# Kernel tuning notes

Measured on AMD Instinct MI355X. Metric: run time of the kernel, lower is better.

## Reference

```python
import jax, jax.numpy as jnp
import numpy as np

N, E = 50000, 800000
HID, EDGE_DIM, HEADS = 128, 16, 4
C = HID // HEADS  # 32
NEG_SLOPE = 0.2  # GATv2Conv default negative_slope


def setup_inputs() -> dict:
    key = jax.random.key(0)
    ks = jax.random.split(key, 16)
    def glorot(k, shape):
        fan_in = shape[0]
        return jax.random.normal(k, shape, jnp.float32) / np.sqrt(fan_in)
    return {
        "x": jax.random.normal(ks[0], (N, HID), jnp.float32),
        "edge_index": jax.random.randint(ks[1], (2, E), 0, N, jnp.int64 if jax.config.jax_enable_x64 else jnp.int32),
        "edge_attr": jax.random.normal(ks[2], (E, EDGE_DIM), jnp.float32),
        # GATv2Conv params (lin_l, lin_r with bias; lin_edge bias-free; att; final bias)
        "Wl": glorot(ks[3], (HID, HID)),
        "bl": jnp.zeros((HID,), jnp.float32),
        "Wr": glorot(ks[4], (HID, HID)),
        "br": jnp.zeros((HID,), jnp.float32),
        "We": glorot(ks[5], (EDGE_DIM, HID)),
        "att": glorot(ks[6], (HEADS, C)),
        "bias_gat": jnp.zeros((HID,), jnp.float32),
        # RMSNorm weights
        "w_norm1": jnp.ones((HID,), jnp.float32),
        "w_norm2": jnp.ones((HID,), jnp.float32),
        # FFN params
        "ffn_w1": glorot(ks[7], (HID, 4 * HID)),
        "ffn_b1": jnp.zeros((4 * HID,), jnp.float32),
        "ffn_w2": glorot(ks[8], (4 * HID, HID)),
        "ffn_b2": jnp.zeros((HID,), jnp.float32),
    }


def rmsnorm(x, w):
    # torch.nn.RMSNorm with eps=None -> eps = finfo(dtype).eps
    eps = jnp.finfo(x.dtype).eps
    ms = jnp.mean(x * x, axis=-1, keepdims=True)
    return x * jax.lax.rsqrt(ms + eps) * w


def gatv2_conv(x, edge_index, edge_attr, Wl, bl, Wr, br, We, att, bias_gat):
    n = x.shape[0]
    h, c = att.shape
    xl = (x @ Wl + bl).reshape(n, h, c)   # source-side transform (x_j)
    xr = (x @ Wr + br).reshape(n, h, c)   # target-side transform (x_i)
    src, dst = edge_index[0], edge_index[1]
    e = (edge_attr @ We).reshape(-1, h, c)
    m = xl[src] + xr[dst] + e                       # [E, H, C] per-edge message pre-activation
    s = jnp.where(m > 0, m, NEG_SLOPE * m)          # LeakyReLU(0.2)
    logits = jnp.einsum('ehc,hc->eh', s, att)       # [E, H]
    # scatter-softmax over edges grouped by target node
    lmax = jax.ops.segment_max(logits, dst, num_segments=n)
    ex = jnp.exp(logits - lmax[dst])
    den = jax.ops.segment_sum(ex, dst, num_segments=n)
    alpha = ex / (den[dst] + 1e-16)                 # PyG softmax denominator guard
    out = jax.ops.segment_sum(alpha[..., None] * xl[src], dst, num_segments=n)
    return out.reshape(n, h * c) + bias_gat


def reference(x, edge_index, edge_attr, Wl, bl, Wr, br, We, att, bias_gat,
              w_norm1, w_norm2, ffn_w1, ffn_b1, ffn_w2, ffn_b2):
    x_attn = gatv2_conv(x, edge_index, edge_attr, Wl, bl, Wr, br, We, att, bias_gat)
    h = rmsnorm(x + x_attn, w_norm1)
    f = jax.nn.gelu(h @ ffn_w1 + ffn_b1, approximate=False) @ ffn_w2 + ffn_b2
    return rmsnorm(h + f, w_norm2)
```

## Files before the change

kernel.cpp:

```cpp
#include <hip/hip_runtime.h>

#define NN 50000
#define EE 800000

typedef unsigned short u16;

#define OFF_EAH  0u
#define OFF_XLH  6400000u
#define OFF_XRH  9600000u
#define OFF_SE   12800000u
#define OFF_CNT  14400000u
#define OFF_OFS  14450000u
#define OFF_WLRT 16000000u
#define OFF_W1T  16016384u
#define OFF_W2T  16049152u

#define RMS_EPS 1.1920928955078125e-7f

typedef float f32x4v __attribute__((ext_vector_type(4)));
typedef short s16x8 __attribute__((ext_vector_type(8)));
typedef _Float16 h16x2 __attribute__((ext_vector_type(2)));
typedef __fp16   g16x2 __attribute__((ext_vector_type(2)));

__device__ __forceinline__ f32x4v mfma16(s16x8 a, s16x8 b, f32x4v c) {
  return __builtin_amdgcn_mfma_f32_16x16x32_bf16(a, b, c, 0, 0, 0);
}
__device__ __forceinline__ u16 f2b(float f) {
  unsigned int u = __float_as_uint(f);
  unsigned int r = (u + 0x7fffu + ((u >> 16) & 1u)) >> 16;
  return (u16)r;
}
__device__ __forceinline__ u16 f2h(float f) {
  union { _Float16 h; u16 u; } x; x.h = (_Float16)f; return x.u;
}
__device__ __forceinline__ h16x2 pk(float a, float b) {
  union { g16x2 g; h16x2 h; } u; u.g = __builtin_amdgcn_cvt_pkrtz(a, b); return u.h;
}
__device__ __forceinline__ h16x2 u2h(unsigned int u) {
  union { unsigned int i; h16x2 h; } x; x.i = u; return x.h;
}
__device__ __forceinline__ unsigned int h2u(h16x2 h) {
  union { unsigned int i; h16x2 h; } x; x.h = h; return x.i;
}
__device__ __forceinline__ float fdot2(h16x2 a, h16x2 b, float c) {
  union { h16x2 h; g16x2 g; } ua, ub; ua.h = a; ub.h = b;
  return __builtin_amdgcn_fdot2(ua.g, ub.g, c, false);
}
__device__ __forceinline__ s16x8 ld_bf16x8_f32(const float* p) {
  float4 v0 = *(const float4*)p;
  float4 v1 = *(const float4*)(p + 4);
  s16x8 r;
  r[0] = (short)f2b(v0.x); r[1] = (short)f2b(v0.y);
  r[2] = (short)f2b(v0.z); r[3] = (short)f2b(v0.w);
  r[4] = (short)f2b(v1.x); r[5] = (short)f2b(v1.y);
  r[6] = (short)f2b(v1.z); r[7] = (short)f2b(v1.w);
  return r;
}
__device__ __forceinline__ int readlane_i32(int v, int lane) {
  return __builtin_amdgcn_readlane(v, lane);
}
__device__ __forceinline__ float gelu_fast(float x) {
  float x2 = x * x;
  float y = x * fmaf(0.07135481283f, x2, 1.5957691216f);
  float e = __expf(-y);
  return x * __builtin_amdgcn_rcpf(1.0f + e);
}

__global__ __launch_bounds__(256) void k_prep(const float* __restrict__ Wl, const float* __restrict__ Wr,
    const float* __restrict__ W1, const float* __restrict__ W2,
    int* __restrict__ cnt, u16* __restrict__ wlrt, u16* __restrict__ w1t, u16* __restrict__ w2t)
{
  int i = blockIdx.x * 256 + threadIdx.x;
  if (i < NN) cnt[i] = 0;
  if (i < 32768) {
    int n = i >> 7, k = i & 127;
    float v = (n < 128) ? Wl[k * 128 + n] : Wr[k * 128 + (n - 128)];
    wlrt[i] = f2b(v);
  }
  {
    int n = i >> 7, k = i & 127;
    w1t[i] = f2b(W1[k * 512 + n]);
  }
  {
    int n = i >> 9, k = i & 511;
    w2t[i] = f2b(W2[k * 128 + n]);
  }
}

__global__ __launch_bounds__(256) void k_hist(const int* __restrict__ ei, const float* __restrict__ eattr,
    int* __restrict__ cnt, unsigned int* __restrict__ eah)
{
  int e = blockIdx.x * 256 + threadIdx.x;
  if (e < EE) {
    atomicAdd(&cnt[ei[EE + e]], 1);
    const float4* src = (const float4*)(eattr + (size_t)e * 16);
    float4 v0 = src[0], v1 = src[1], v2 = src[2], v3 = src[3];
    uint4 o0, o1;
    o0.x = h2u(pk(v0.x, v0.y));
    o0.y = h2u(pk(v0.z, v0.w));
    o0.z = h2u(pk(v1.x, v1.y));
    o0.w = h2u(pk(v1.z, v1.w));
    o1.x = h2u(pk(v2.x, v2.y));
    o1.y = h2u(pk(v2.z, v2.w));
    o1.z = h2u(pk(v3.x, v3.y));
    o1.w = h2u(pk(v3.z, v3.w));
    uint4* dst = (uint4*)(eah + (size_t)e * 8);
    dst[0] = o0; dst[1] = o1;
  }
}

__global__ __launch_bounds__(1024) void k_scan(const int* __restrict__ cnt,
    int* __restrict__ offs, int* __restrict__ pos)
{
  __shared__ int wsum[16];
  __shared__ int carry_s;
  int tid = threadIdx.x, lane = tid & 63, wv = tid >> 6;
  if (tid == 0) carry_s = 0;
  __syncthreads();
  for (int base = 0; base < NN; base += 1024) {
    int i = base + tid;
    int v = (i < NN) ? cnt[i] : 0;
    int x = v;
#pragma unroll
    for (int ofs = 1; ofs < 64; ofs <<= 1) {
      int y = __shfl_up(x, ofs);
      if (lane >= ofs) x += y;
    }
    if (lane == 63) wsum[wv] = x;
    __syncthreads();
    if (wv == 0) {
      int s = (lane < 16) ? wsum[lane] : 0;
#pragma unroll
      for (int ofs = 1; ofs < 16; ofs <<= 1) {
        int y = __shfl_up(s, ofs);
        if (lane >= ofs) s += y;
      }
      if (lane < 16) wsum[lane] = s;
    }
    __syncthreads();
    int wbase = (wv > 0) ? wsum[wv - 1] : 0;
    int incl = x + wbase + carry_s;
    if (i < NN) { offs[i + 1] = incl; pos[i] = incl - v; }
    if (base == 0 && tid == 0) offs[0] = 0;
    __syncthreads();
    if (tid == 1023) carry_s = incl;
    __syncthreads();
  }
}

__global__ __launch_bounds__(256) void k_permute(const int* __restrict__ ei,
    int* __restrict__ pos, int2* __restrict__ se)
{
  int e = blockIdx.x * 256 + threadIdx.x;
  if (e < EE) {
    int slot = atomicAdd(&pos[ei[EE + e]], 1);
    se[slot] = make_int2(ei[e], e);
  }
}

__global__ __launch_bounds__(256) void k1_mfma(const float* __restrict__ x, const u16* __restrict__ wlrt,
    const float* __restrict__ bl, const float* __restrict__ br,
    u16* __restrict__ xlh, u16* __restrict__ xrh)
{
  int tid = threadIdx.x;
  int w = tid >> 6, lane = tid & 63;
  int quad = lane >> 4, l16 = lane & 15;
  int row0 = blockIdx.x * 32;
  int ko = quad * 8;
  f32x4v acc[2][4];
#pragma unroll
  for (int mt = 0; mt < 2; ++mt)
#pragma unroll
    for (int nt = 0; nt < 4; ++nt) acc[mt][nt] = (f32x4v){0.f, 0.f, 0.f, 0.f};
#pragma unroll
  for (int ks = 0; ks < 4; ++ks) {
    int k0 = ks * 32 + ko;
    s16x8 a[2];
#pragma unroll
    for (int mt = 0; mt < 2; ++mt) {
      int row = row0 + mt * 16 + l16; if (row >= NN) row = NN - 1;
      a[mt] = ld_bf16x8_f32(x + row * 128 + k0);
    }
#pragma unroll
    for (int nt = 0; nt < 4; ++nt) {
      int col = w * 64 + nt * 16 + l16;
      s16x8 b = *(const s16x8*)(wlrt + col * 128 + k0);
      acc[0][nt] = mfma16(a[0], b, acc[0][nt]);
      acc[1][nt] = mfma16(a[1], b, acc[1][nt]);
    }
  }
#pragma unroll
  for (int nt = 0; nt < 4; ++nt) {
    int col = w * 64 + nt * 16 + l16;
    bool isl = col < 128;
    float bias = isl ? bl[col] : br[col - 128];
    u16* dst = isl ? xlh : xrh;
    int cc = isl ? col : col - 128;
#pragma unroll
    for (int mt = 0; mt < 2; ++mt)
#pragma unroll
      for (int r = 0; r < 4; ++r) {
        int row = row0 + mt * 16 + quad * 4 + r;
        if (row < NN) dst[row * 128 + cc] = f2h(acc[mt][nt][r] + bias);
      }
  }
}

__global__ __launch_bounds__(256) void kA_attn(
    const int* __restrict__ offs, const int2* __restrict__ se,
    const unsigned int* __restrict__ eah,
    const float* __restrict__ att, const float* __restrict__ We,
    const u16* __restrict__ xlh, const u16* __restrict__ xrh,
    const float* __restrict__ x, const float* __restrict__ bg,
    const float* __restrict__ wn1, float* __restrict__ h)
{
  int l = threadIdx.x & 63;
  int wid = (blockIdx.x * blockDim.x + threadIdx.x) >> 6;
  int nw = (gridDim.x * blockDim.x) >> 6;
  int c0 = 2 * l;

  h16x2 wefA[8], wefB[8];
#pragma unroll
  for (int k = 0; k < 8; ++k) {
    wefA[k] = pk(We[(2 * k) * 128 + c0], We[(2 * k + 1) * 128 + c0]);
    wefB[k] = pk(We[(2 * k) * 128 + c0 + 1], We[(2 * k + 1) * 128 + c0 + 1]);
  }
  h16x2 att2 = pk(att[c0], att[c0 + 1]);
  const h16x2 c06 = {(_Float16)0.6f, (_Float16)0.6f};
  const h16x2 c04 = {(_Float16)0.4f, (_Float16)0.4f};

  int myj = l >> 3, myk = l & 7;

  for (int d = wid; d < NN; d += nw) {
    int start = offs[d];
    int deg = offs[d + 1] - start;
    h16x2 xr2 = u2h(*(const unsigned int*)(xrh + (size_t)d * 128 + c0));
    float mh = -1e30f, lh = 0.f, O0 = 0.f, O1 = 0.f;

    for (int base = 0; base < deg; base += 64) {
      bool act = (base + l) < deg;
      int idx = start + base + l;
      int2 sev = act ? se[idx] : make_int2(0, 0);
      int cnt = min(64, deg - base);
      for (int sub8 = 0; sub8 < cnt; sub8 += 8) {
        int eidq = __shfl(sev.y, sub8 + myj);
        unsigned int eav = eah[(size_t)eidq * 8 + myk];

        float p[8];
        unsigned int xlu[8];
#pragma unroll
        for (int j = 0; j < 8; ++j) {
          float ep0 = 0.f, ep1 = 0.f;
#pragma unroll
          for (int k = 0; k < 8; ++k) {
            unsigned int ev = (unsigned int)readlane_i32((int)eav, j * 8 + k);
            h16x2 e2 = u2h(ev);
            ep0 = fdot2(e2, wefA[k], ep0);
            ep1 = fdot2(e2, wefB[k], ep1);
          }
          int sr = readlane_i32(sev.x, sub8 + j);
          unsigned int xv = *(const unsigned int*)(xlh + (size_t)sr * 128 + c0);
          xlu[j] = xv;
          h16x2 m2 = u2h(xv) + xr2 + pk(ep0, ep1);
          h16x2 am = u2h(h2u(m2) & 0x7FFF7FFFu);
          h16x2 s2 = m2 * c06 + am * c04;
          p[j] = fdot2(s2, att2, 0.f);
        }
#pragma unroll
        for (int o = 1; o <= 8; o <<= 1) {
          p[0] += __shfl_xor(p[0], o); p[1] += __shfl_xor(p[1], o);
          p[2] += __shfl_xor(p[2], o); p[3] += __shfl_xor(p[3], o);
          p[4] += __shfl_xor(p[4], o); p[5] += __shfl_xor(p[5], o);
          p[6] += __shfl_xor(p[6], o); p[7] += __shfl_xor(p[7], o);
        }
#pragma unroll
        for (int j = 0; j < 8; ++j) if (sub8 + j >= cnt) p[j] = -1e30f;
        float nm = fmaxf(fmaxf(fmaxf(p[0], p[1]), fmaxf(p[2], p[3])),
                         fmaxf(fmaxf(p[4], p[5]), fmaxf(p[6], p[7])));
        nm = fmaxf(nm, mh);
        float sc = __expf(mh - nm);
#pragma unroll
        for (int j = 0; j < 8; ++j) p[j] = __expf(p[j] - nm);
        float bs = ((p[0] + p[1]) + (p[2] + p[3])) + ((p[4] + p[5]) + (p[6] + p[7]));
        lh = fmaf(lh, sc, bs);
        O0 *= sc; O1 *= sc;
        mh = nm;
#pragma unroll
        for (int j = 0; j < 8; ++j) {
          h16x2 xl2 = u2h(xlu[j]);
          O0 = fmaf(p[j], (float)xl2.x, O0);
          O1 = fmaf(p[j], (float)xl2.y, O1);
        }
      }
    }
    float inv = 1.f / (lh + 1e-16f);
    float2 xu = *(const float2*)(x + (size_t)d * 128 + c0);
    float2 bu = *(const float2*)(bg + c0);
    float v0 = O0 * inv + xu.x + bu.x;
    float v1 = O1 * inv + xu.y + bu.y;
    float ss = v0 * v0 + v1 * v1;
#pragma unroll
    for (int o = 1; o < 64; o <<= 1) ss += __shfl_xor(ss, o);
    float rr = rsqrtf(ss * (1.f / 128.f) + RMS_EPS);
    float2 wu = *(const float2*)(wn1 + c0);
    *(float2*)(h + (size_t)d * 128 + c0) = make_float2(v0 * rr * wu.x, v1 * rr * wu.y);
  }
}

__device__ __forceinline__ u16* tls_addr(u16* tls, int row, int col) {
  int byte = (row << 10) + (col << 1);
  byte ^= (row & 7) << 4;
  return (u16*)((char*)tls + byte);
}

__global__ __launch_bounds__(512) void k6_mfma(const float* h,
    const u16* __restrict__ w1t, const u16* __restrict__ w2t,
    const float* __restrict__ b1, const float* __restrict__ b2,
    const float* __restrict__ wn2, float* out)
{
  __shared__ u16 tls[32 * 512];
  int tid = threadIdx.x;
  int w = tid >> 6, lane = tid & 63;
  int quad = lane >> 4, l16 = lane & 15;
  int row0 = blockIdx.x * 32;
  int ko = quad * 8;

  f32x4v acc1[2][4];
#pragma unroll
  for (int mt = 0; mt < 2; ++mt)
#pragma unroll
    for (int nt = 0; nt < 4; ++nt) acc1[mt][nt] = (f32x4v){0.f, 0.f, 0.f, 0.f};
#pragma unroll
  for (int ks = 0; ks < 4; ++ks) {
    int k0 = ks * 32 + ko;
    s16x8 a[2];
#pragma unroll
    for (int mt = 0; mt < 2; ++mt) {
      int row = row0 + mt * 16 + l16; if (row >= NN) row = NN - 1;
      a[mt] = ld_bf16x8_f32(h + row * 128 + k0);
    }
#pragma unroll
    for (int nt = 0; nt < 4; ++nt) {
      int col = w * 64 + nt * 16 + l16;
      s16x8 b = *(const s16x8*)(w1t + col * 128 + k0);
      acc1[0][nt] = mfma16(a[0], b, acc1[0][nt]);
      acc1[1][nt] = mfma16(a[1], b, acc1[1][nt]);
    }
  }
#pragma unroll
  for (int nt = 0; nt < 4; ++nt) {
    int col = w * 64 + nt * 16 + l16;
    float bb = b1[col];
#pragma unroll
    for (int mt = 0; mt < 2; ++mt)
#pragma unroll
      for (int r = 0; r < 4; ++r) {
        float t = gelu_fast(acc1[mt][nt][r] + bb);
        *tls_addr(tls, mt * 16 + quad * 4 + r, col) = f2b(t);
      }
  }
  __syncthreads();

  f32x4v acc2[2];
  acc2[0] = (f32x4v){0.f, 0.f, 0.f, 0.f};
  acc2[1] = (f32x4v){0.f, 0.f, 0.f, 0.f};
  int col = w * 16 + l16;
  const u16* bptr = w2t + col * 512;
#pragma unroll
  for (int ks = 0; ks < 16; ++ks) {
    int k0 = ks * 32 + ko;
    s16x8 a2[2];
#pragma unroll
    for (int mt = 0; mt < 2; ++mt)
      a2[mt] = *(const s16x8*)tls_addr(tls, mt * 16 + l16, k0);
    s16x8 b = *(const s16x8*)(bptr + k0);
    acc2[0] = mfma16(a2[0], b, acc2[0]);
    acc2[1] = mfma16(a2[1], b, acc2[1]);
  }

  float bb2 = b2[col], wn = wn2[col];
  float ov[2][4];
#pragma unroll
  for (int mt = 0; mt < 2; ++mt)
#pragma unroll
    for (int r = 0; r < 4; ++r) {
      int row = row0 + mt * 16 + quad * 4 + r;
      int rowc = row < NN ? row : NN - 1;
      ov[mt][r] = h[rowc * 128 + col] + acc2[mt][r] + bb2;
    }
  __syncthreads();
  float (*red)[32] = (float (*)[32])(void*)tls;
#pragma unroll
  for (int mt = 0; mt < 2; ++mt)
#pragma unroll
    for (int r = 0; r < 4; ++r) {
      float q = ov[mt][r] * ov[mt][r];
      q += __shfl_xor(q, 1); q += __shfl_xor(q, 2);
      q += __shfl_xor(q, 4); q += __shfl_xor(q, 8);
      if (l16 == 0) red[w][mt * 16 + quad * 4 + r] = q;
    }
  __syncthreads();
#pragma unroll
  for (int mt = 0; mt < 2; ++mt)
#pragma unroll
    for (int r = 0; r < 4; ++r) {
      int rl = mt * 16 + quad * 4 + r;
      float tot = ((red[0][rl] + red[1][rl]) + (red[2][rl] + red[3][rl]))
                + ((red[4][rl] + red[5][rl]) + (red[6][rl] + red[7][rl]));
      float rr = rsqrtf(tot * (1.f / 128.f) + RMS_EPS);
      int row = row0 + rl;
      if (row < NN) {
        out[row * 128 + col] = ov[mt][r] * rr * wn;
      }
    }
}

extern "C" void kernel_launch(void* const* d_in, const int* in_sizes, int n_in,
                              void* d_out, int out_size, void* d_ws, size_t ws_size,
                              hipStream_t stream) {
  const float* x   = (const float*)d_in[0];
  const int*   ei  = (const int*)d_in[1];
  const float* ea  = (const float*)d_in[2];
  const float* Wl  = (const float*)d_in[3];
  const float* bl  = (const float*)d_in[4];
  const float* Wr  = (const float*)d_in[5];
  const float* br  = (const float*)d_in[6];
  const float* We  = (const float*)d_in[7];
  const float* att = (const float*)d_in[8];
  const float* bg  = (const float*)d_in[9];
  const float* wn1 = (const float*)d_in[10];
  const float* wn2 = (const float*)d_in[11];
  const float* W1  = (const float*)d_in[12];
  const float* b1  = (const float*)d_in[13];
  const float* W2  = (const float*)d_in[14];
  const float* b2  = (const float*)d_in[15];

  float* wsf = (float*)d_ws;
  int*   wsi = (int*)d_ws;

  unsigned int* eah = (unsigned int*)(wsf + OFF_EAH);
  u16* xlh    = (u16*)(wsf + OFF_XLH);
  u16* xrh    = (u16*)(wsf + OFF_XRH);
  int2* se    = (int2*)(wsf + OFF_SE);
  int* cnt    = wsi + OFF_CNT;
  int* pos    = wsi + OFF_CNT;
  int* offs   = wsi + OFF_OFS;
  u16* wlrt   = (u16*)(wsf + OFF_WLRT);
  u16* w1t    = (u16*)(wsf + OFF_W1T);
  u16* w2t    = (u16*)(wsf + OFF_W2T);
  float* hbuf = (float*)d_out;

  k_prep<<<256, 256, 0, stream>>>(Wl, Wr, W1, W2, cnt, wlrt, w1t, w2t);

  k_hist<<<(EE + 255) / 256, 256, 0, stream>>>(ei, ea, cnt, eah);
  k_scan<<<1, 1024, 0, stream>>>(cnt, offs, pos);
  k_permute<<<(EE + 255) / 256, 256, 0, stream>>>(ei, pos, se);

  k1_mfma<<<(NN + 31) / 32, 256, 0, stream>>>(x, wlrt, bl, br, xlh, xrh);

  kA_attn<<<2048, 256, 0, stream>>>(offs, se, eah, att, We, xlh, xrh, x, bg, wn1, hbuf);

  k6_mfma<<<(NN + 31) / 32, 512, 0, stream>>>(hbuf, w1t, w2t, b1, b2, wn2, (float*)d_out);
}
```

Measured before the change: 508.1 us.

## Parallelize scan per-thread, load edge attrs as uint4, fold LeakyReLU into att, double grid

The single-block scan now gives each thread a contiguous chunk of 49 counts and does one block-wide scan, replacing the 49-iteration loop with its barriers. In the attention kernel, each edge's fp16 attributes are read with uniform-address uint4 loads instead of a per-lane load followed by 64 readlanes. The LeakyReLU constants are folded into pre-scaled attention vectors, saving a multiply-add per edge. The attention grid is doubled for more waves in flight, at the cost of higher register pressure from the 16 uint4 buffers.

```diff
diff --git a/kernel.cpp b/kernel.cpp
--- a/kernel.cpp
+++ b/kernel.cpp
@@ -109,43 +109,51 @@
   }
 }
 
+#define SCAN_PER 49
 __global__ __launch_bounds__(1024) void k_scan(const int* __restrict__ cnt,
     int* __restrict__ offs, int* __restrict__ pos)
 {
   __shared__ int wsum[16];
-  __shared__ int carry_s;
   int tid = threadIdx.x, lane = tid & 63, wv = tid >> 6;
-  if (tid == 0) carry_s = 0;
+  int base = tid * SCAN_PER;
+  int v[SCAN_PER];
+  int s = 0;
+#pragma unroll
+  for (int i = 0; i < SCAN_PER; ++i) {
+    int idx = base + i;
+    v[i] = (idx < NN) ? cnt[idx] : 0;
+    s += v[i];
+  }
+  int x = s;
+#pragma unroll
+  for (int o = 1; o < 64; o <<= 1) {
+    int y = __shfl_up(x, o);
+    if (lane >= o) x += y;
+  }
+  if (lane == 63) wsum[wv] = x;
   __syncthreads();
-  for (int base = 0; base < NN; base += 1024) {
-    int i = base + tid;
-    int v = (i < NN) ? cnt[i] : 0;
-    int x = v;
-#pragma unroll
-    for (int ofs = 1; ofs < 64; ofs <<= 1) {
-      int y = __shfl_up(x, ofs);
-      if (lane >= ofs) x += y;
-    }
-    if (lane == 63) wsum[wv] = x;
-    __syncthreads();
-    if (wv == 0) {
-      int s = (lane < 16) ? wsum[lane] : 0;
-#pragma unroll
-      for (int ofs = 1; ofs < 16; ofs <<= 1) {
-        int y = __shfl_up(s, ofs);
-        if (lane >= ofs) s += y;
-      }
-      if (lane < 16) wsum[lane] = s;
-    }
-    __syncthreads();
-    int wbase = (wv > 0) ? wsum[wv - 1] : 0;
-    int incl = x + wbase + carry_s;
-    if (i < NN) { offs[i + 1] = incl; pos[i] = incl - v; }
-    if (base == 0 && tid == 0) offs[0] = 0;
-    __syncthreads();
-    if (tid == 1023) carry_s = incl;
-    __syncthreads();
-  }
+  if (wv == 0) {
+    int t = (lane < 16) ? wsum[lane] : 0;
+#pragma unroll
+    for (int o = 1; o < 16; o <<= 1) {
+      int y = __shfl_up(t, o);
+      if (lane >= o) t += y;
+    }
+    if (lane < 16) wsum[lane] = t;
+  }
+  __syncthreads();
+  int wbase = (wv > 0) ? wsum[wv - 1] : 0;
+  int run = x - s + wbase;
+#pragma unroll
+  for (int i = 0; i < SCAN_PER; ++i) {
+    int idx = base + i;
+    if (idx < NN) {
+      pos[idx] = run;
+      run += v[i];
+      offs[idx + 1] = run;
+    }
+  }
+  if (tid == 0) offs[0] = 0;
 }
 
 __global__ __launch_bounds__(256) void k_permute(const int* __restrict__ ei,
@@ -225,11 +233,9 @@
     wefA[k] = pk(We[(2 * k) * 128 + c0], We[(2 * k + 1) * 128 + c0]);
     wefB[k] = pk(We[(2 * k) * 128 + c0 + 1], We[(2 * k + 1) * 128 + c0 + 1]);
   }
-  h16x2 att2 = pk(att[c0], att[c0 + 1]);
-  const h16x2 c06 = {(_Float16)0.6f, (_Float16)0.6f};
-  const h16x2 c04 = {(_Float16)0.4f, (_Float16)0.4f};
-
-  int myj = l >> 3, myk = l & 7;
+  float a0 = att[c0], a1 = att[c0 + 1];
+  h16x2 att06 = pk(0.6f * a0, 0.6f * a1);
+  h16x2 att04 = pk(0.4f * a0, 0.4f * a1);
 
   for (int d = wid; d < NN; d += nw) {
     int start = offs[d];
@@ -243,28 +249,34 @@
       int2 sev = act ? se[idx] : make_int2(0, 0);
       int cnt = min(64, deg - base);
       for (int sub8 = 0; sub8 < cnt; sub8 += 8) {
-        int eidq = __shfl(sev.y, sub8 + myj);
-        unsigned int eav = eah[(size_t)eidq * 8 + myk];
+        uint4 ea0[8], ea1[8];
+#pragma unroll
+        for (int j = 0; j < 8; ++j) {
+          int eid = readlane_i32(sev.y, sub8 + j);
+          const uint4* p8 = (const uint4*)(eah + (size_t)(unsigned)eid * 8);
+          ea0[j] = p8[0]; ea1[j] = p8[1];
+        }
 
         float p[8];
         unsigned int xlu[8];
 #pragma unroll
         for (int j = 0; j < 8; ++j) {
           float ep0 = 0.f, ep1 = 0.f;
-#pragma unroll
-          for (int k = 0; k < 8; ++k) {
-            unsigned int ev = (unsigned int)readlane_i32((int)eav, j * 8 + k);
-            h16x2 e2 = u2h(ev);
-            ep0 = fdot2(e2, wefA[k], ep0);
-            ep1 = fdot2(e2, wefB[k], ep1);
-          }
+          ep0 = fdot2(u2h(ea0[j].x), wefA[0], ep0); ep1 = fdot2(u2h(ea0[j].x), wefB[0], ep1);
+          ep0 = fdot2(u2h(ea0[j].y), wefA[1], ep0); ep1 = fdot2(u2h(ea0[j].y), wefB[1], ep1);
+          ep0 = fdot2(u2h(ea0[j].z), wefA[2], ep0); ep1 = fdot2(u2h(ea0[j].z), wefB[2], ep1);
+          ep0 = fdot2(u2h(ea0[j].w), wefA[3], ep0); ep1 = fdot2(u2h(ea0[j].w), wefB[3], ep1);
+          ep0 = fdot2(u2h(ea1[j].x), wefA[4], ep0); ep1 = fdot2(u2h(ea1[j].x), wefB[4], ep1);
+          ep0 = fdot2(u2h(ea1[j].y), wefA[5], ep0); ep1 = fdot2(u2h(ea1[j].y), wefB[5], ep1);
+          ep0 = fdot2(u2h(ea1[j].z), wefA[6], ep0); ep1 = fdot2(u2h(ea1[j].z), wefB[6], ep1);
+          ep0 = fdot2(u2h(ea1[j].w), wefA[7], ep0); ep1 = fdot2(u2h(ea1[j].w), wefB[7], ep1);
+
           int sr = readlane_i32(sev.x, sub8 + j);
           unsigned int xv = *(const unsigned int*)(xlh + (size_t)sr * 128 + c0);
           xlu[j] = xv;
           h16x2 m2 = u2h(xv) + xr2 + pk(ep0, ep1);
           h16x2 am = u2h(h2u(m2) & 0x7FFF7FFFu);
-          h16x2 s2 = m2 * c06 + am * c04;
-          p[j] = fdot2(s2, att2, 0.f);
+          p[j] = fdot2(m2, att06, fdot2(am, att04, 0.f));
         }
 #pragma unroll
         for (int o = 1; o <= 8; o <<= 1) {
@@ -458,7 +470,7 @@
 
   k1_mfma<<<(NN + 31) / 32, 256, 0, stream>>>(x, wlrt, bl, br, xlh, xrh);
 
-  kA_attn<<<2048, 256, 0, stream>>>(offs, se, eah, att, We, xlh, xrh, x, bg, wn1, hbuf);
+  kA_attn<<<4096, 256, 0, stream>>>(offs, se, eah, att, We, xlh, xrh, x, bg, wn1, hbuf);
 
   k6_mfma<<<(NN + 31) / 32, 512, 0, stream>>>(hbuf, w1t, w2t, b1, b2, wn2, (float*)d_out);
 }
```

Measured after the change: 517.1 us. About the same (+1.8%).
